# Kernel tuning notes

Hardware: AMD Instinct MI355X
Metric: run time of the kernel (lower is better)

Reference implementation:

```python
import jax, jax.numpy as jnp
import numpy as np

B, I, H, WR, UR = 4096, 512, 1024, 128, 128

def setup_inputs() -> dict:
    key = jax.random.key(0)
    ks = jax.random.split(key, 12)
    inp = {
        "x": jax.random.normal(ks[0], (B, I), jnp.float32),
        "h": jax.random.normal(ks[1], (B, H), jnp.float32),
        "c": jax.random.normal(ks[2], (B, H), jnp.float32),
        "U_x": 0.1 * jax.random.normal(ks[3], (I, WR), jnp.float32),
        "U_h": 0.1 * jax.random.normal(ks[4], (H, UR), jnp.float32),
        "V_x": 0.1 * jax.random.normal(ks[5], (4 * H, WR), jnp.float32),
        "V_h": 0.1 * jax.random.normal(ks[6], (4 * H, UR), jnp.float32),
        "b_x": 0.1 * jax.random.normal(ks[7], (4 * H,), jnp.float32),
        "b_h": 0.1 * jax.random.normal(ks[8], (4 * H,), jnp.float32),
        "dia_x": 0.1 * jax.random.normal(ks[9], (1, I), jnp.float32),
        "dia_h": 0.1 * jax.random.normal(ks[10], (1, H), jnp.float32),
    }
    return inp

def reference(x, h, c, U_x, U_h, V_x, V_h, b_x, b_h, dia_x, dia_h):
    b, i = x.shape
    hid = h.shape[1]
    # low-rank GEMMs: [B,4H]
    lowered_x = (x @ U_x) @ V_x.T
    lowered_h = (h @ U_h) @ V_h.T
    # per-gate diagonal corrections (vectorized over the 4 gates)
    V_x4 = V_x.reshape(4, hid, -1)          # [4,H,WR]
    corr_x = jnp.sum(U_x[None] * V_x4[:, :i, :], axis=-1)   # [4,I]
    vm_refined_x = x[:, None, :] * corr_x[None]              # [B,4,I]
    vm_refined_x = jnp.pad(vm_refined_x, ((0, 0), (0, 0), (0, hid - i))).reshape(b, 4 * hid)
    V_h4 = V_h.reshape(4, hid, -1)          # [4,H,UR]
    corr_h = jnp.sum(U_h[None] * V_h4, axis=-1)              # [4,H]
    vm_refined_h = (h[:, None, :] * corr_h[None]).reshape(b, 4 * hid)
    gx = lowered_x - vm_refined_x + b_x
    gh = lowered_h - vm_refined_h + b_h
    # diagonal (vector-multiplication) terms, x-part zero-padded to hidden size
    vm_x = jnp.pad(dia_x * x, ((0, 0), (0, hid - i)))        # [B,H]
    vm_h = dia_h * h                                          # [B,H]
    add = vm_x + vm_h
    xi, xf, xo, xn = jnp.split(gx, 4, axis=1)
    hi, hf, ho, hn = jnp.split(gh, 4, axis=1)
    inputgate = jax.nn.sigmoid(xi + hi + add)
    forgetgate = jax.nn.sigmoid(xf + hf + add)
    outputgate = jax.nn.sigmoid(xo + ho + add)
    newgate = jnp.tanh(xn + hn + add)
    c_next = forgetgate * c + inputgate * newgate
    h_next = outputgate * jnp.tanh(c_next)
    return (h_next, c_next)
```

## Files before the change

kernel.cpp:

```cpp
#include <hip/hip_runtime.h>

#define BB 4096
#define II 512
#define HH 1024
#define RR 128

typedef __bf16 bf16x8 __attribute__((ext_vector_type(8)));
typedef float  f32x4  __attribute__((ext_vector_type(4)));
typedef unsigned short u16x8 __attribute__((ext_vector_type(8)));
typedef unsigned short u16x4 __attribute__((ext_vector_type(4)));

__device__ __forceinline__ unsigned short f2bf(float f) {
  unsigned int u = __float_as_uint(f);
  u += 0x7fffu + ((u >> 16) & 1u);
  return (unsigned short)(u >> 16);
}
__device__ __forceinline__ float sigm(float v) { return 1.f / (1.f + __expf(-v)); }
__device__ __forceinline__ float tanh_f(float v) { return 1.f - 2.f / (1.f + __expf(2.f * v)); }


__global__ __launch_bounds__(256) void prep_kernel(
    const float* __restrict__ Ux, const float* __restrict__ Uh,
    const float* __restrict__ Vx, const float* __restrict__ Vh,
    const float* __restrict__ bx, const float* __restrict__ bh,
    unsigned short* __restrict__ VC, unsigned short* __restrict__ UTX,
    unsigned short* __restrict__ UTH, float* __restrict__ CX,
    float* __restrict__ CH, float* __restrict__ BC)
{
  int tid = blockIdx.x * 256 + threadIdx.x;
  if (tid < 131072) {
    int row = tid >> 5, kc = tid & 31, k = kc * 8;
    int jb = row >> 7;
    int t7 = row & 127;
    int w = t7 >> 5, f = (t7 >> 4) & 1, cc = t7 & 15;
    int g = f * 2 + (cc >> 3);
    int j = jb * 32 + w * 8 + (cc & 7);
    int vrow = g * HH + j;
    const float* src = (k < 128) ? (Vx + vrow * RR + k) : (Vh + vrow * RR + (k - 128));
    f32x4 a = *(const f32x4*)src;
    f32x4 b = *(const f32x4*)(src + 4);
    u16x8 o;
    o[0]=f2bf(a[0]); o[1]=f2bf(a[1]); o[2]=f2bf(a[2]); o[3]=f2bf(a[3]);
    o[4]=f2bf(b[0]); o[5]=f2bf(b[1]); o[6]=f2bf(b[2]); o[7]=f2bf(b[3]);
    *(u16x8*)(VC + row * 256 + k) = o;
  } else if (tid < 139264) {
    int idx = tid - 131072;
    int n = idx & 127, k = (idx >> 7) * 8;
    u16x8 o;
    #pragma unroll
    for (int e = 0; e < 8; ++e) o[e] = f2bf(Ux[(k + e) * RR + n]);
    *(u16x8*)(UTX + n * II + k) = o;
  } else if (tid < 155648) {
    int idx = tid - 139264;
    int n = idx & 127, k = (idx >> 7) * 8;
    u16x8 o;
    #pragma unroll
    for (int e = 0; e < 8; ++e) o[e] = f2bf(Uh[(k + e) * RR + n]);
    *(u16x8*)(UTH + n * HH + k) = o;
  } else if (tid < 157696) {
    int idx = tid - 155648;
    int g = idx >> 9, i = idx & 511;
    const float* u = Ux + i * RR;
    const float* v = Vx + (g * HH + i) * RR;
    float s = 0.f;
    #pragma unroll 8
    for (int r4 = 0; r4 < 32; ++r4) {
      f32x4 uu = *(const f32x4*)(u + r4 * 4);
      f32x4 vv = *(const f32x4*)(v + r4 * 4);
      s += uu[0]*vv[0] + uu[1]*vv[1] + uu[2]*vv[2] + uu[3]*vv[3];
    }
    CX[g * II + i] = s;
  } else if (tid < 161792) {
    int idx = tid - 157696;
    int g = idx >> 10, j = idx & 1023;
    const float* u = Uh + j * RR;
    const float* v = Vh + (g * HH + j) * RR;
    float s = 0.f;
    #pragma unroll 8
    for (int r4 = 0; r4 < 32; ++r4) {
      f32x4 uu = *(const f32x4*)(u + r4 * 4);
      f32x4 vv = *(const f32x4*)(v + r4 * 4);
      s += uu[0]*vv[0] + uu[1]*vv[1] + uu[2]*vv[2] + uu[3]*vv[3];
    }
    CH[g * HH + j] = s;
  } else if (tid < 165888) {
    int n = tid - 161792;
    BC[n] = bx[n] + bh[n];
  }
}

template<int K, int NKS>
__device__ __forceinline__ void s1_core(
    const float* __restrict__ src, const unsigned short* __restrict__ Ut,
    unsigned short* __restrict__ T, float* __restrict__ Red,
    int b0, int p, int t)
{
  int l = t & 63, w = t >> 6;
  int row = l & 15, kof = (l >> 4) * 8;
  int kc0 = w * (K / 4);
  const float* ap = src + (b0 + row) * K + kc0 + kof;
  const unsigned short* bp = Ut + row * K + kc0 + kof;

  f32x4 acc[8];
  #pragma unroll
  for (int fi = 0; fi < 8; ++fi) acc[fi] = (f32x4){0.f, 0.f, 0.f, 0.f};

  #pragma unroll
  for (int ks = 0; ks < NKS; ++ks) {
    f32x4 a0 = *(const f32x4*)(ap + ks * 32);
    f32x4 a1 = *(const f32x4*)(ap + ks * 32 + 4);
    union { bf16x8 v; unsigned short u[8]; } af;
    af.u[0]=f2bf(a0[0]); af.u[1]=f2bf(a0[1]); af.u[2]=f2bf(a0[2]); af.u[3]=f2bf(a0[3]);
    af.u[4]=f2bf(a1[0]); af.u[5]=f2bf(a1[1]); af.u[6]=f2bf(a1[2]); af.u[7]=f2bf(a1[3]);
    #pragma unroll
    for (int fi = 0; fi < 8; ++fi) {
      bf16x8 bf = *(const bf16x8*)(bp + fi * 16 * K + ks * 32);
      acc[fi] = __builtin_amdgcn_mfma_f32_16x16x32_bf16(af.v, bf, acc[fi], 0, 0, 0);
    }
  }

  #pragma unroll
  for (int fi = 0; fi < 8; ++fi) {
    int n = fi * 16 + row;
    #pragma unroll
    for (int reg = 0; reg < 4; ++reg) {
      int m = (l >> 4) * 4 + reg;
      Red[(w * 16 + m) * 132 + n] = acc[fi][reg];
    }
  }
  __syncthreads();

  #pragma unroll
  for (int it = 0; it < 2; ++it) {
    int q = it * 256 + t;
    int m = q >> 5, c4 = (q & 31) * 4;
    f32x4 s0 = *(const f32x4*)(Red + (0 * 16 + m) * 132 + c4);
    f32x4 s1 = *(const f32x4*)(Red + (1 * 16 + m) * 132 + c4);
    f32x4 s2 = *(const f32x4*)(Red + (2 * 16 + m) * 132 + c4);
    f32x4 s3 = *(const f32x4*)(Red + (3 * 16 + m) * 132 + c4);
    f32x4 s = s0 + s1 + s2 + s3;
    u16x4 o;
    o[0]=f2bf(s[0]); o[1]=f2bf(s[1]); o[2]=f2bf(s[2]); o[3]=f2bf(s[3]);
    *(u16x4*)(T + (b0 + m) * 256 + p * 128 + c4) = o;
  }
}

__global__ __launch_bounds__(256) void stage1_kernel(
    const float* __restrict__ x, const float* __restrict__ h,
    const unsigned short* __restrict__ UTX, const unsigned short* __restrict__ UTH,
    unsigned short* __restrict__ T)
{
  __shared__ alignas(16) float Red[4 * 16 * 132];
  int t = threadIdx.x;
  int mb = blockIdx.x & 255;
  if (blockIdx.x < 256) s1_core<II, II / 128>(x, UTX, T, Red, mb * 16, 0, t);
  else                  s1_core<HH, HH / 128>(h, UTH, T, Red, mb * 16, 1, t);
}

__global__ __launch_bounds__(256) void stage2_kernel(
    const unsigned short* __restrict__ T, const unsigned short* __restrict__ VC,
    const float* __restrict__ CX, const float* __restrict__ CH, const float* __restrict__ BC,
    const float* __restrict__ x, const float* __restrict__ h, const float* __restrict__ c,
    const float* __restrict__ dx, const float* __restrict__ dh,
    float* __restrict__ out)
{
  __shared__ alignas(16) unsigned short As[64 * 256];
  int t = threadIdx.x, l = t & 63, w = t >> 6;
  int xcd = blockIdx.x & 7, bi = blockIdx.x >> 3;
  int jb = xcd * 4 + (bi >> 6);
  int mb = bi & 63;
  int b0 = mb * 64, j0 = jb * 32;
  int r16 = l & 15, hi = l >> 4;
  int koff = hi * 8;
  int ch = (l >> 3) & 1;
  int jv = j0 + w * 8 + (l & 7);
  bool has_x = (j0 < II);

  #pragma unroll
  for (int p = 0; p < 8; ++p) {
    int G = p * 256 + t;
    int r = G >> 5, gl = G & 31;
    int gs = gl ^ (r & 7);
    const unsigned short* gp = T + (b0 + r) * 256 + gs * 8;
    __builtin_amdgcn_global_load_lds(
        (const __attribute__((address_space(1))) void*)gp,
        (__attribute__((address_space(3))) void*)(As + G * 8), 16, 0, 0);
  }

  float hv[8], cv[8], xv[8];
  #pragma unroll
  for (int rf = 0; rf < 4; ++rf)
    #pragma unroll
    for (int rr = 0; rr < 2; ++rr) {
      int q = rf * 2 + rr;
      int b = b0 + rf * 16 + hi * 4 + ch * 2 + rr;
      hv[q] = h[b * HH + jv];
      cv[q] = c[b * HH + jv];
      xv[q] = has_x ? x[b * II + jv] : 0.f;
    }

  const unsigned short* vp = VC + (jb * 128 + w * 32 + r16) * 256 + koff;
  bf16x8 bf0[8], bf1[8];
  #pragma unroll
  for (int ks = 0; ks < 8; ++ks) {
    bf0[ks] = *(const bf16x8*)(vp + ks * 32);
    bf1[ks] = *(const bf16x8*)(vp + 16 * 256 + ks * 32);
  }

  float dhv = dh[jv];
  float dxv = has_x ? dx[jv] : 0.f;
  float cxv0 = has_x ? CX[0 * II + jv] : 0.f;
  float cxv1 = has_x ? CX[1 * II + jv] : 0.f;
  float cxv2 = has_x ? CX[2 * II + jv] : 0.f;
  float cxv3 = has_x ? CX[3 * II + jv] : 0.f;
  float chv0 = CH[0 * HH + jv], chv1 = CH[1 * HH + jv];
  float chv2 = CH[2 * HH + jv], chv3 = CH[3 * HH + jv];
  float bcv0 = BC[0 * HH + jv], bcv1 = BC[1 * HH + jv];
  float bcv2 = BC[2 * HH + jv], bcv3 = BC[3 * HH + jv];

  asm volatile("s_waitcnt vmcnt(0)" ::: "memory");
  __syncthreads();

  const char* Ab = (const char*)As;
  int rbase = r16 * 512;

  #pragma unroll
  for (int rf = 0; rf < 4; ++rf) {
    f32x4 acc0 = (f32x4){0.f, 0.f, 0.f, 0.f};
    f32x4 acc1 = (f32x4){0.f, 0.f, 0.f, 0.f};
    #pragma unroll
    for (int ks = 0; ks < 8; ++ks) {
      int gsw = ((ks * 4 + hi) ^ (r16 & 7)) * 16;
      bf16x8 a = *(const bf16x8*)(Ab + rf * 8192 + rbase + gsw);
      acc0 = __builtin_amdgcn_mfma_f32_16x16x32_bf16(a, bf0[ks], acc0, 0, 0, 0);
      acc1 = __builtin_amdgcn_mfma_f32_16x16x32_bf16(a, bf1[ks], acc1, 0, 0, 0);
    }
    #pragma unroll
    for (int rr = 0; rr < 2; ++rr) {
      int q = rf * 2 + rr;
      float keep0 = ch ? acc0[2 + rr] : acc0[rr];
      float send0 = ch ? acc0[rr] : acc0[2 + rr];
      float keep1 = ch ? acc1[2 + rr] : acc1[rr];
      float send1 = ch ? acc1[rr] : acc1[2 + rr];
      float recv0 = __shfl_xor(send0, 8);
      float recv1 = __shfl_xor(send1, 8);
      float p0 = ch ? recv0 : keep0;
      float p1 = ch ? keep0 : recv0;
      float p2 = ch ? recv1 : keep1;
      float p3 = ch ? keep1 : recv1;
      int b = b0 + rf * 16 + hi * 4 + ch * 2 + rr;
      float hvq = hv[q], cvq = cv[q];
      float addv = dhv * hvq;
      if (has_x) {
        float xvq = xv[q];
        addv += dxv * xvq;
        p0 -= xvq * cxv0; p1 -= xvq * cxv1; p2 -= xvq * cxv2; p3 -= xvq * cxv3;
      }
      p0 += bcv0 + addv - hvq * chv0;
      p1 += bcv1 + addv - hvq * chv1;
      p2 += bcv2 + addv - hvq * chv2;
      p3 += bcv3 + addv - hvq * chv3;
      float ig = sigm(p0);
      float fg = sigm(p1);
      float og = sigm(p2);
      float ng = tanh_f(p3);
      float cn = fg * cvq + ig * ng;
      float hn = og * tanh_f(cn);
      out[b * HH + jv] = hn;
      out[BB * HH + b * HH + jv] = cn;
    }
  }
}

extern "C" void kernel_launch(void* const* d_in, const int* in_sizes, int n_in,
                              void* d_out, int out_size, void* d_ws, size_t ws_size,
                              hipStream_t stream) {
  const float* x  = (const float*)d_in[0];
  const float* h  = (const float*)d_in[1];
  const float* c  = (const float*)d_in[2];
  const float* Ux = (const float*)d_in[3];
  const float* Uh = (const float*)d_in[4];
  const float* Vx = (const float*)d_in[5];
  const float* Vh = (const float*)d_in[6];
  const float* bx = (const float*)d_in[7];
  const float* bh = (const float*)d_in[8];
  const float* dx = (const float*)d_in[9];
  const float* dh = (const float*)d_in[10];
  char* ws = (char*)d_ws;
  unsigned short* T   = (unsigned short*)(ws + 0);
  unsigned short* VC  = (unsigned short*)(ws + 2097152);
  unsigned short* UTX = (unsigned short*)(ws + 4194304);
  unsigned short* UTH = (unsigned short*)(ws + 4325376);
  float* CX = (float*)(ws + 4587520);
  float* CH = (float*)(ws + 4595712);
  float* BC = (float*)(ws + 4612096);
  float* out = (float*)d_out;

  prep_kernel<<<648, 256, 0, stream>>>(Ux, Uh, Vx, Vh, bx, bh, VC, UTX, UTH, CX, CH, BC);
  stage1_kernel<<<512, 256, 0, stream>>>(x, h, UTX, UTH, T);
  stage2_kernel<<<2048, 256, 0, stream>>>(T, VC, CX, CH, BC, x, h, c, dx, dh, out);
}
```

Baseline: 65.41 us.

## Double-buffer stage2 over four batch tiles and widen stage1 split-K to eight waves

Stage2 now launches a quarter as many blocks, and each block handles four consecutive 64-row batch tiles. The V weight fragments and per-column constants are loaded once per block, and LDS is double-buffered so the load of the next T tile and its h/c/x prefetch overlap the MFMA and gate math of the current tile. Stage1 moves to 512-thread blocks with an 8-way K split, with all A loads hoisted ahead of the MFMA loop, to expose more memory parallelism. The cost is more LDS per block, higher register pressure from the two sets of prefetch arrays, and fewer stage2 blocks to fill the GPU.

```diff
diff --git a/kernel.cpp b/kernel.cpp
--- a/kernel.cpp
+++ b/kernel.cpp
@@ -97,21 +97,28 @@
 {
   int l = t & 63, w = t >> 6;
   int row = l & 15, kof = (l >> 4) * 8;
-  int kc0 = w * (K / 4);
+  int kc0 = w * (K / 8);
   const float* ap = src + (b0 + row) * K + kc0 + kof;
   const unsigned short* bp = Ut + row * K + kc0 + kof;
 
+  f32x4 a0[NKS], a1[NKS];
+  #pragma unroll
+  for (int ks = 0; ks < NKS; ++ks) {
+    a0[ks] = *(const f32x4*)(ap + ks * 32);
+    a1[ks] = *(const f32x4*)(ap + ks * 32 + 4);
+  }
+
   f32x4 acc[8];
   #pragma unroll
   for (int fi = 0; fi < 8; ++fi) acc[fi] = (f32x4){0.f, 0.f, 0.f, 0.f};
 
   #pragma unroll
   for (int ks = 0; ks < NKS; ++ks) {
-    f32x4 a0 = *(const f32x4*)(ap + ks * 32);
-    f32x4 a1 = *(const f32x4*)(ap + ks * 32 + 4);
     union { bf16x8 v; unsigned short u[8]; } af;
-    af.u[0]=f2bf(a0[0]); af.u[1]=f2bf(a0[1]); af.u[2]=f2bf(a0[2]); af.u[3]=f2bf(a0[3]);
-    af.u[4]=f2bf(a1[0]); af.u[5]=f2bf(a1[1]); af.u[6]=f2bf(a1[2]); af.u[7]=f2bf(a1[3]);
+    af.u[0]=f2bf(a0[ks][0]); af.u[1]=f2bf(a0[ks][1]);
+    af.u[2]=f2bf(a0[ks][2]); af.u[3]=f2bf(a0[ks][3]);
+    af.u[4]=f2bf(a1[ks][0]); af.u[5]=f2bf(a1[ks][1]);
+    af.u[6]=f2bf(a1[ks][2]); af.u[7]=f2bf(a1[ks][3]);
     #pragma unroll
     for (int fi = 0; fi < 8; ++fi) {
       bf16x8 bf = *(const bf16x8*)(bp + fi * 16 * K + ks * 32);
@@ -130,52 +137,31 @@
   }
   __syncthreads();
 
-  #pragma unroll
-  for (int it = 0; it < 2; ++it) {
-    int q = it * 256 + t;
-    int m = q >> 5, c4 = (q & 31) * 4;
-    f32x4 s0 = *(const f32x4*)(Red + (0 * 16 + m) * 132 + c4);
-    f32x4 s1 = *(const f32x4*)(Red + (1 * 16 + m) * 132 + c4);
-    f32x4 s2 = *(const f32x4*)(Red + (2 * 16 + m) * 132 + c4);
-    f32x4 s3 = *(const f32x4*)(Red + (3 * 16 + m) * 132 + c4);
-    f32x4 s = s0 + s1 + s2 + s3;
-    u16x4 o;
-    o[0]=f2bf(s[0]); o[1]=f2bf(s[1]); o[2]=f2bf(s[2]); o[3]=f2bf(s[3]);
-    *(u16x4*)(T + (b0 + m) * 256 + p * 128 + c4) = o;
-  }
-}
-
-__global__ __launch_bounds__(256) void stage1_kernel(
+  int m = t >> 5, c4 = (t & 31) * 4;
+  f32x4 s = (f32x4){0.f, 0.f, 0.f, 0.f};
+  #pragma unroll
+  for (int wp = 0; wp < 8; ++wp)
+    s += *(const f32x4*)(Red + (wp * 16 + m) * 132 + c4);
+  u16x4 o;
+  o[0]=f2bf(s[0]); o[1]=f2bf(s[1]); o[2]=f2bf(s[2]); o[3]=f2bf(s[3]);
+  *(u16x4*)(T + (b0 + m) * 256 + p * 128 + c4) = o;
+}
+
+__global__ __launch_bounds__(512) void stage1_kernel(
     const float* __restrict__ x, const float* __restrict__ h,
     const unsigned short* __restrict__ UTX, const unsigned short* __restrict__ UTH,
     unsigned short* __restrict__ T)
 {
-  __shared__ alignas(16) float Red[4 * 16 * 132];
+  __shared__ alignas(16) float Red[8 * 16 * 132];
   int t = threadIdx.x;
   int mb = blockIdx.x & 255;
-  if (blockIdx.x < 256) s1_core<II, II / 128>(x, UTX, T, Red, mb * 16, 0, t);
-  else                  s1_core<HH, HH / 128>(h, UTH, T, Red, mb * 16, 1, t);
-}
-
-__global__ __launch_bounds__(256) void stage2_kernel(
-    const unsigned short* __restrict__ T, const unsigned short* __restrict__ VC,
-    const float* __restrict__ CX, const float* __restrict__ CH, const float* __restrict__ BC,
-    const float* __restrict__ x, const float* __restrict__ h, const float* __restrict__ c,
-    const float* __restrict__ dx, const float* __restrict__ dh,
-    float* __restrict__ out)
-{
-  __shared__ alignas(16) unsigned short As[64 * 256];
-  int t = threadIdx.x, l = t & 63, w = t >> 6;
-  int xcd = blockIdx.x & 7, bi = blockIdx.x >> 3;
-  int jb = xcd * 4 + (bi >> 6);
-  int mb = bi & 63;
-  int b0 = mb * 64, j0 = jb * 32;
-  int r16 = l & 15, hi = l >> 4;
-  int koff = hi * 8;
-  int ch = (l >> 3) & 1;
-  int jv = j0 + w * 8 + (l & 7);
-  bool has_x = (j0 < II);
-
+  if (blockIdx.x < 256) s1_core<II, II / 256>(x, UTX, T, Red, mb * 16, 0, t);
+  else                  s1_core<HH, HH / 256>(h, UTH, T, Red, mb * 16, 1, t);
+}
+
+__device__ __forceinline__ void s2_stage(unsigned short* Asb,
+    const unsigned short* __restrict__ T, int b0, int t)
+{
   #pragma unroll
   for (int p = 0; p < 8; ++p) {
     int G = p * 256 + t;
@@ -184,10 +170,14 @@
     const unsigned short* gp = T + (b0 + r) * 256 + gs * 8;
     __builtin_amdgcn_global_load_lds(
         (const __attribute__((address_space(1))) void*)gp,
-        (__attribute__((address_space(3))) void*)(As + G * 8), 16, 0, 0);
-  }
-
-  float hv[8], cv[8], xv[8];
+        (__attribute__((address_space(3))) void*)(Asb + G * 8), 16, 0, 0);
+  }
+}
+
+__device__ __forceinline__ void s2_pref(float (&hv)[8], float (&cv)[8], float (&xv)[8],
+    const float* __restrict__ h, const float* __restrict__ c,
+    const float* __restrict__ x, int b0, int hi, int ch, int jv, bool has_x)
+{
   #pragma unroll
   for (int rf = 0; rf < 4; ++rf)
     #pragma unroll
@@ -198,32 +188,17 @@
       cv[q] = c[b * HH + jv];
       xv[q] = has_x ? x[b * II + jv] : 0.f;
     }
-
-  const unsigned short* vp = VC + (jb * 128 + w * 32 + r16) * 256 + koff;
-  bf16x8 bf0[8], bf1[8];
-  #pragma unroll
-  for (int ks = 0; ks < 8; ++ks) {
-    bf0[ks] = *(const bf16x8*)(vp + ks * 32);
-    bf1[ks] = *(const bf16x8*)(vp + 16 * 256 + ks * 32);
-  }
-
-  float dhv = dh[jv];
-  float dxv = has_x ? dx[jv] : 0.f;
-  float cxv0 = has_x ? CX[0 * II + jv] : 0.f;
-  float cxv1 = has_x ? CX[1 * II + jv] : 0.f;
-  float cxv2 = has_x ? CX[2 * II + jv] : 0.f;
-  float cxv3 = has_x ? CX[3 * II + jv] : 0.f;
-  float chv0 = CH[0 * HH + jv], chv1 = CH[1 * HH + jv];
-  float chv2 = CH[2 * HH + jv], chv3 = CH[3 * HH + jv];
-  float bcv0 = BC[0 * HH + jv], bcv1 = BC[1 * HH + jv];
-  float bcv2 = BC[2 * HH + jv], bcv3 = BC[3 * HH + jv];
-
-  asm volatile("s_waitcnt vmcnt(0)" ::: "memory");
-  __syncthreads();
-
-  const char* Ab = (const char*)As;
+}
+
+__device__ __forceinline__ void s2_comp(const unsigned short* Asb,
+    const bf16x8 (&bf0)[8], const bf16x8 (&bf1)[8],
+    const float (&hv)[8], const float (&cv)[8], const float (&xv)[8],
+    float dhv, float dxv, const f32x4& cxv, const f32x4& chv, const f32x4& bcv,
+    int b0, int r16, int hi, int ch, int jv, bool has_x,
+    float* __restrict__ out)
+{
+  const char* Ab = (const char*)Asb;
   int rbase = r16 * 512;
-
   #pragma unroll
   for (int rf = 0; rf < 4; ++rf) {
     f32x4 acc0 = (f32x4){0.f, 0.f, 0.f, 0.f};
@@ -254,12 +229,13 @@
       if (has_x) {
         float xvq = xv[q];
         addv += dxv * xvq;
-        p0 -= xvq * cxv0; p1 -= xvq * cxv1; p2 -= xvq * cxv2; p3 -= xvq * cxv3;
+        p0 -= xvq * cxv[0]; p1 -= xvq * cxv[1];
+        p2 -= xvq * cxv[2]; p3 -= xvq * cxv[3];
       }
-      p0 += bcv0 + addv - hvq * chv0;
-      p1 += bcv1 + addv - hvq * chv1;
-      p2 += bcv2 + addv - hvq * chv2;
-      p3 += bcv3 + addv - hvq * chv3;
+      p0 += bcv[0] + addv - hvq * chv[0];
+      p1 += bcv[1] + addv - hvq * chv[1];
+      p2 += bcv[2] + addv - hvq * chv[2];
+      p3 += bcv[3] + addv - hvq * chv[3];
       float ig = sigm(p0);
       float fg = sigm(p1);
       float og = sigm(p2);
@@ -270,6 +246,78 @@
       out[BB * HH + b * HH + jv] = cn;
     }
   }
+}
+
+#define S2_SYNC() do { \
+    asm volatile("s_waitcnt vmcnt(0)" ::: "memory"); \
+    __syncthreads(); \
+  } while (0)
+
+__global__ __launch_bounds__(256) void stage2_kernel(
+    const unsigned short* __restrict__ T, const unsigned short* __restrict__ VC,
+    const float* __restrict__ CX, const float* __restrict__ CH, const float* __restrict__ BC,
+    const float* __restrict__ x, const float* __restrict__ h, const float* __restrict__ c,
+    const float* __restrict__ dx, const float* __restrict__ dh,
+    float* __restrict__ out)
+{
+  __shared__ alignas(16) unsigned short As0[64 * 256];
+  __shared__ alignas(16) unsigned short As1[64 * 256];
+  int t = threadIdx.x, l = t & 63, w = t >> 6;
+  int xcd = blockIdx.x & 7, i = blockIdx.x >> 3;
+  int jb = xcd * 4 + (i >> 4);
+  int ms = i & 15;
+  int j0 = jb * 32;
+  int r16 = l & 15, hi = l >> 4, koff = hi * 8, ch = (l >> 3) & 1;
+  int jv = j0 + w * 8 + (l & 7);
+  bool has_x = (j0 < II);
+  int mb0 = ms * 4;
+
+  s2_stage(As0, T, (mb0 + 0) * 64, t);
+  float hA[8], cA[8], xA[8], hB[8], cB[8], xB[8];
+  s2_pref(hA, cA, xA, h, c, x, (mb0 + 0) * 64, hi, ch, jv, has_x);
+
+  const unsigned short* vp = VC + (jb * 128 + w * 32 + r16) * 256 + koff;
+  bf16x8 bf0[8], bf1[8];
+  #pragma unroll
+  for (int ks = 0; ks < 8; ++ks) {
+    bf0[ks] = *(const bf16x8*)(vp + ks * 32);
+    bf1[ks] = *(const bf16x8*)(vp + 16 * 256 + ks * 32);
+  }
+
+  float dhv = dh[jv];
+  float dxv = has_x ? dx[jv] : 0.f;
+  f32x4 cxv = (f32x4){0.f, 0.f, 0.f, 0.f}, chv, bcv;
+  if (has_x) {
+    cxv[0] = CX[jv]; cxv[1] = CX[II + jv];
+    cxv[2] = CX[2 * II + jv]; cxv[3] = CX[3 * II + jv];
+  }
+  chv[0] = CH[jv]; chv[1] = CH[HH + jv];
+  chv[2] = CH[2 * HH + jv]; chv[3] = CH[3 * HH + jv];
+  bcv[0] = BC[jv]; bcv[1] = BC[HH + jv];
+  bcv[2] = BC[2 * HH + jv]; bcv[3] = BC[3 * HH + jv];
+
+  S2_SYNC();
+
+  s2_stage(As1, T, (mb0 + 1) * 64, t);
+  s2_pref(hB, cB, xB, h, c, x, (mb0 + 1) * 64, hi, ch, jv, has_x);
+  s2_comp(As0, bf0, bf1, hA, cA, xA, dhv, dxv, cxv, chv, bcv,
+          (mb0 + 0) * 64, r16, hi, ch, jv, has_x, out);
+  S2_SYNC();
+
+  s2_stage(As0, T, (mb0 + 2) * 64, t);
+  s2_pref(hA, cA, xA, h, c, x, (mb0 + 2) * 64, hi, ch, jv, has_x);
+  s2_comp(As1, bf0, bf1, hB, cB, xB, dhv, dxv, cxv, chv, bcv,
+          (mb0 + 1) * 64, r16, hi, ch, jv, has_x, out);
+  S2_SYNC();
+
+  s2_stage(As1, T, (mb0 + 3) * 64, t);
+  s2_pref(hB, cB, xB, h, c, x, (mb0 + 3) * 64, hi, ch, jv, has_x);
+  s2_comp(As0, bf0, bf1, hA, cA, xA, dhv, dxv, cxv, chv, bcv,
+          (mb0 + 2) * 64, r16, hi, ch, jv, has_x, out);
+  S2_SYNC();
+
+  s2_comp(As1, bf0, bf1, hB, cB, xB, dhv, dxv, cxv, chv, bcv,
+          (mb0 + 3) * 64, r16, hi, ch, jv, has_x, out);
 }
 
 extern "C" void kernel_launch(void* const* d_in, const int* in_sizes, int n_in,
@@ -297,6 +345,6 @@
   float* out = (float*)d_out;
 
   prep_kernel<<<648, 256, 0, stream>>>(Ux, Uh, Vx, Vh, bx, bh, VC, UTX, UTH, CX, CH, BC);
-  stage1_kernel<<<512, 256, 0, stream>>>(x, h, UTX, UTH, T);
-  stage2_kernel<<<2048, 256, 0, stream>>>(T, VC, CX, CH, BC, x, h, c, dx, dh, out);
-}
+  stage1_kernel<<<512, 512, 0, stream>>>(x, h, UTX, UTH, T);
+  stage2_kernel<<<512, 256, 0, stream>>>(T, VC, CX, CH, BC, x, h, c, dx, dh, out);
+}
```

Result: faster. 62.37 us (-4.6%).

## Widen stage1 K-split to 8 waves and overlap stage2 loads with partial waitcnt

Applied to the files above, without the earlier changes.

Stage1 now runs 512 threads per block, splitting K across 8 waves, and issues all A-row loads up front before the MFMA loop. The cross-wave reduction in shared memory grows to 8 partials. Stage2 reorders its loads so the LDS copy and B-fragment loads are issued first, then waits with a partial vmcnt instead of vmcnt(0). It also replaces the has_x branch with a multiply-by-mask and adds an occupancy hint through launch_bounds. The partial vmcnt count depends on exact load ordering, which is fragile: if the count is wrong the kernel could read LDS or registers before their data arrives.

```diff
diff --git a/kernel.cpp b/kernel.cpp
--- a/kernel.cpp
+++ b/kernel.cpp
@@ -97,21 +97,28 @@
 {
   int l = t & 63, w = t >> 6;
   int row = l & 15, kof = (l >> 4) * 8;
-  int kc0 = w * (K / 4);
+  int kc0 = w * (K / 8);
   const float* ap = src + (b0 + row) * K + kc0 + kof;
   const unsigned short* bp = Ut + row * K + kc0 + kof;
 
+  f32x4 a0[NKS], a1[NKS];
+  #pragma unroll
+  for (int ks = 0; ks < NKS; ++ks) {
+    a0[ks] = *(const f32x4*)(ap + ks * 32);
+    a1[ks] = *(const f32x4*)(ap + ks * 32 + 4);
+  }
+
   f32x4 acc[8];
   #pragma unroll
   for (int fi = 0; fi < 8; ++fi) acc[fi] = (f32x4){0.f, 0.f, 0.f, 0.f};
 
   #pragma unroll
   for (int ks = 0; ks < NKS; ++ks) {
-    f32x4 a0 = *(const f32x4*)(ap + ks * 32);
-    f32x4 a1 = *(const f32x4*)(ap + ks * 32 + 4);
     union { bf16x8 v; unsigned short u[8]; } af;
-    af.u[0]=f2bf(a0[0]); af.u[1]=f2bf(a0[1]); af.u[2]=f2bf(a0[2]); af.u[3]=f2bf(a0[3]);
-    af.u[4]=f2bf(a1[0]); af.u[5]=f2bf(a1[1]); af.u[6]=f2bf(a1[2]); af.u[7]=f2bf(a1[3]);
+    af.u[0]=f2bf(a0[ks][0]); af.u[1]=f2bf(a0[ks][1]);
+    af.u[2]=f2bf(a0[ks][2]); af.u[3]=f2bf(a0[ks][3]);
+    af.u[4]=f2bf(a1[ks][0]); af.u[5]=f2bf(a1[ks][1]);
+    af.u[6]=f2bf(a1[ks][2]); af.u[7]=f2bf(a1[ks][3]);
     #pragma unroll
     for (int fi = 0; fi < 8; ++fi) {
       bf16x8 bf = *(const bf16x8*)(bp + fi * 16 * K + ks * 32);
@@ -130,34 +137,29 @@
   }
   __syncthreads();
 
-  #pragma unroll
-  for (int it = 0; it < 2; ++it) {
-    int q = it * 256 + t;
-    int m = q >> 5, c4 = (q & 31) * 4;
-    f32x4 s0 = *(const f32x4*)(Red + (0 * 16 + m) * 132 + c4);
-    f32x4 s1 = *(const f32x4*)(Red + (1 * 16 + m) * 132 + c4);
-    f32x4 s2 = *(const f32x4*)(Red + (2 * 16 + m) * 132 + c4);
-    f32x4 s3 = *(const f32x4*)(Red + (3 * 16 + m) * 132 + c4);
-    f32x4 s = s0 + s1 + s2 + s3;
-    u16x4 o;
-    o[0]=f2bf(s[0]); o[1]=f2bf(s[1]); o[2]=f2bf(s[2]); o[3]=f2bf(s[3]);
-    *(u16x4*)(T + (b0 + m) * 256 + p * 128 + c4) = o;
-  }
-}
-
-__global__ __launch_bounds__(256) void stage1_kernel(
+  int m = t >> 5, c4 = (t & 31) * 4;
+  f32x4 s = (f32x4){0.f, 0.f, 0.f, 0.f};
+  #pragma unroll
+  for (int wp = 0; wp < 8; ++wp)
+    s += *(const f32x4*)(Red + (wp * 16 + m) * 132 + c4);
+  u16x4 o;
+  o[0]=f2bf(s[0]); o[1]=f2bf(s[1]); o[2]=f2bf(s[2]); o[3]=f2bf(s[3]);
+  *(u16x4*)(T + (b0 + m) * 256 + p * 128 + c4) = o;
+}
+
+__global__ __launch_bounds__(512) void stage1_kernel(
     const float* __restrict__ x, const float* __restrict__ h,
     const unsigned short* __restrict__ UTX, const unsigned short* __restrict__ UTH,
     unsigned short* __restrict__ T)
 {
-  __shared__ alignas(16) float Red[4 * 16 * 132];
+  __shared__ alignas(16) float Red[8 * 16 * 132];
   int t = threadIdx.x;
   int mb = blockIdx.x & 255;
-  if (blockIdx.x < 256) s1_core<II, II / 128>(x, UTX, T, Red, mb * 16, 0, t);
-  else                  s1_core<HH, HH / 128>(h, UTH, T, Red, mb * 16, 1, t);
-}
-
-__global__ __launch_bounds__(256) void stage2_kernel(
+  if (blockIdx.x < 256) s1_core<II, II / 256>(x, UTX, T, Red, mb * 16, 0, t);
+  else                  s1_core<HH, HH / 256>(h, UTH, T, Red, mb * 16, 1, t);
+}
+
+__global__ __launch_bounds__(256, 5) void stage2_kernel(
     const unsigned short* __restrict__ T, const unsigned short* __restrict__ VC,
     const float* __restrict__ CX, const float* __restrict__ CH, const float* __restrict__ BC,
     const float* __restrict__ x, const float* __restrict__ h, const float* __restrict__ c,
@@ -170,11 +172,11 @@
   int jb = xcd * 4 + (bi >> 6);
   int mb = bi & 63;
   int b0 = mb * 64, j0 = jb * 32;
-  int r16 = l & 15, hi = l >> 4;
-  int koff = hi * 8;
-  int ch = (l >> 3) & 1;
+  int r16 = l & 15, hi = l >> 4, koff = hi * 8, ch = (l >> 3) & 1;
   int jv = j0 + w * 8 + (l & 7);
   bool has_x = (j0 < II);
+  int jx = has_x ? jv : (jv - II);
+  float fx = has_x ? 1.f : 0.f;
 
   #pragma unroll
   for (int p = 0; p < 8; ++p) {
@@ -186,6 +188,25 @@
         (const __attribute__((address_space(1))) void*)gp,
         (__attribute__((address_space(3))) void*)(As + G * 8), 16, 0, 0);
   }
+  asm volatile("" ::: "memory");
+
+  const unsigned short* vp = VC + (jb * 128 + w * 32 + r16) * 256 + koff;
+  bf16x8 bf0[8], bf1[8];
+  #pragma unroll
+  for (int ks = 0; ks < 8; ++ks) {
+    bf0[ks] = *(const bf16x8*)(vp + ks * 32);
+    bf1[ks] = *(const bf16x8*)(vp + 16 * 256 + ks * 32);
+  }
+
+  float dhv = dh[jv];
+  float dxv = fx * dx[jx];
+  f32x4 cxv, chv, bcv;
+  cxv[0] = fx * CX[jx];          cxv[1] = fx * CX[II + jx];
+  cxv[2] = fx * CX[2 * II + jx]; cxv[3] = fx * CX[3 * II + jx];
+  chv[0] = CH[jv]; chv[1] = CH[HH + jv];
+  chv[2] = CH[2 * HH + jv]; chv[3] = CH[3 * HH + jv];
+  bcv[0] = BC[jv]; bcv[1] = BC[HH + jv];
+  bcv[2] = BC[2 * HH + jv]; bcv[3] = BC[3 * HH + jv];
 
   float hv[8], cv[8], xv[8];
   #pragma unroll
@@ -196,30 +217,15 @@
       int b = b0 + rf * 16 + hi * 4 + ch * 2 + rr;
       hv[q] = h[b * HH + jv];
       cv[q] = c[b * HH + jv];
-      xv[q] = has_x ? x[b * II + jv] : 0.f;
-    }
-
-  const unsigned short* vp = VC + (jb * 128 + w * 32 + r16) * 256 + koff;
-  bf16x8 bf0[8], bf1[8];
-  #pragma unroll
-  for (int ks = 0; ks < 8; ++ks) {
-    bf0[ks] = *(const bf16x8*)(vp + ks * 32);
-    bf1[ks] = *(const bf16x8*)(vp + 16 * 256 + ks * 32);
-  }
-
-  float dhv = dh[jv];
-  float dxv = has_x ? dx[jv] : 0.f;
-  float cxv0 = has_x ? CX[0 * II + jv] : 0.f;
-  float cxv1 = has_x ? CX[1 * II + jv] : 0.f;
-  float cxv2 = has_x ? CX[2 * II + jv] : 0.f;
-  float cxv3 = has_x ? CX[3 * II + jv] : 0.f;
-  float chv0 = CH[0 * HH + jv], chv1 = CH[1 * HH + jv];
-  float chv2 = CH[2 * HH + jv], chv3 = CH[3 * HH + jv];
-  float bcv0 = BC[0 * HH + jv], bcv1 = BC[1 * HH + jv];
-  float bcv2 = BC[2 * HH + jv], bcv3 = BC[3 * HH + jv];
-
-  asm volatile("s_waitcnt vmcnt(0)" ::: "memory");
-  __syncthreads();
+      xv[q] = fx * x[b * II + jx];
+    }
+
+  asm volatile("" ::: "memory");
+  asm volatile("s_waitcnt vmcnt(40)" ::: "memory");
+  __builtin_amdgcn_sched_barrier(0);
+  __builtin_amdgcn_s_barrier();
+  __builtin_amdgcn_sched_barrier(0);
+  asm volatile("" ::: "memory");
 
   const char* Ab = (const char*)As;
   int rbase = r16 * 512;
@@ -249,17 +255,12 @@
       float p2 = ch ? recv1 : keep1;
       float p3 = ch ? keep1 : recv1;
       int b = b0 + rf * 16 + hi * 4 + ch * 2 + rr;
-      float hvq = hv[q], cvq = cv[q];
-      float addv = dhv * hvq;
-      if (has_x) {
-        float xvq = xv[q];
-        addv += dxv * xvq;
-        p0 -= xvq * cxv0; p1 -= xvq * cxv1; p2 -= xvq * cxv2; p3 -= xvq * cxv3;
-      }
-      p0 += bcv0 + addv - hvq * chv0;
-      p1 += bcv1 + addv - hvq * chv1;
-      p2 += bcv2 + addv - hvq * chv2;
-      p3 += bcv3 + addv - hvq * chv3;
+      float hvq = hv[q], cvq = cv[q], xvq = xv[q];
+      float addv = dhv * hvq + dxv * xvq;
+      p0 += bcv[0] + addv - hvq * chv[0] - xvq * cxv[0];
+      p1 += bcv[1] + addv - hvq * chv[1] - xvq * cxv[1];
+      p2 += bcv[2] + addv - hvq * chv[2] - xvq * cxv[2];
+      p3 += bcv[3] + addv - hvq * chv[3] - xvq * cxv[3];
       float ig = sigm(p0);
       float fg = sigm(p1);
       float og = sigm(p2);
@@ -297,6 +298,6 @@
   float* out = (float*)d_out;
 
   prep_kernel<<<648, 256, 0, stream>>>(Ux, Uh, Vx, Vh, bx, bh, VC, UTX, UTH, CX, CH, BC);
-  stage1_kernel<<<512, 256, 0, stream>>>(x, h, UTX, UTH, T);
+  stage1_kernel<<<512, 512, 0, stream>>>(x, h, UTX, UTH, T);
   stage2_kernel<<<2048, 256, 0, stream>>>(T, VC, CX, CH, BC, x, h, c, dx, dh, out);
 }
```

New measurement: 131.7 us. 2.01x slower.
